# Kernel tuning notes

Measured on AMD Instinct MI355X. Metric: run time of the kernel, lower is better.

The kernel has to match this reference:

```python
import jax, jax.numpy as jnp
import numpy as np

B, L, D = 32, 2048, 512
DFF = D // 2          # FeedForward d_ff = d_model // 2
NBLK = 2 * 3          # head_number * block_layer sequential TX blocks
EPS = 1e-6


def _norm(x, alpha, bias):
    # torch Norm: alpha*(x-mean)/(std+eps)+bias, std unbiased (ddof=1)
    mu = x.mean(axis=-1, keepdims=True)
    var = ((x - mu) ** 2).sum(axis=-1, keepdims=True) / (x.shape[-1] - 1)
    return alpha * (x - mu) / (jnp.sqrt(var) + EPS) + bias


def setup_inputs() -> dict:
    key = jax.random.key(0)
    ks = jax.random.split(key, 8)
    q = jax.random.normal(ks[0], (B, D), dtype=jnp.float32)
    k = jax.random.normal(ks[1], (B, L, D), dtype=jnp.float32)
    v = jax.random.normal(ks[2], (B, L, D), dtype=jnp.float32)
    # FeedForward params per block, init std=0.001 as in source
    W1 = jax.random.normal(ks[3], (NBLK, D, DFF), dtype=jnp.float32) * 0.001
    b1 = jnp.zeros((NBLK, DFF), dtype=jnp.float32)
    W2 = jax.random.normal(ks[4], (NBLK, DFF, D), dtype=jnp.float32) * 0.001
    b2 = jnp.zeros((NBLK, D), dtype=jnp.float32)
    # Norm params (alpha=1, bias=0 at init)
    alpha1 = jnp.ones((NBLK, D), dtype=jnp.float32)
    bias1 = jnp.zeros((NBLK, D), dtype=jnp.float32)
    alpha2 = jnp.ones((NBLK, D), dtype=jnp.float32)
    bias2 = jnp.zeros((NBLK, D), dtype=jnp.float32)
    return {"q": q, "k": k, "v": v, "W1": W1, "b1": b1, "W2": W2, "b2": b2,
            "alpha1": alpha1, "bias1": bias1, "alpha2": alpha2, "bias2": bias2}


def reference(q, k, v, W1, b1, W2, b2, alpha1, bias1, alpha2, bias2):
    scale = 1.0 / jnp.sqrt(jnp.asarray(D, dtype=q.dtype))
    weights_list = []
    outs = []
    idx = 0
    for _head in range(2):
        for _layer in range(3):
            # attention: scores (B,L) = <q, k_l>/sqrt(D); output (B,D)
            scores = jnp.einsum('bd,bld->bl', q, k) * scale
            s = jax.nn.softmax(scores, axis=-1)
            A = jnp.einsum('bl,bld->bd', s, v)
            q_ = _norm(A + q, alpha1[idx], bias1[idx])
            ff = jax.nn.relu(q_ @ W1[idx] + b1[idx]) @ W2[idx] + b2[idx]
            q = _norm(q_ + ff, alpha2[idx], bias2[idx])
            weights_list.append(s)
            idx += 1
        outs.append(q)
    out = jnp.concatenate(outs, axis=-1)          # head_comb_mode='cat' -> (B, 2D)
    weights = jnp.stack(weights_list, axis=-1)    # (B, L, 6)
    return out, weights
```

## Files before the change

### kernel.cpp

```cpp
#include <hip/hip_runtime.h>

#define BB 32
#define LL 2048
#define DD 512
#define DFFN 256
#define NBLK 6
#define NCHUNK 32
#define CHUNK 64
#define NTHR 256
#define EPSV 1e-6f

typedef float v4f __attribute__((ext_vector_type(4)));
typedef unsigned v2u __attribute__((ext_vector_type(2)));

__device__ __forceinline__ float bflo(unsigned u){ return __uint_as_float(u << 16); }
__device__ __forceinline__ float bfhi(unsigned u){ return __uint_as_float(u & 0xFFFF0000u); }
__device__ __forceinline__ unsigned pack2bf(float lo, float hi){
  unsigned a = __float_as_uint(lo); a += 0x7FFFu + ((a >> 16) & 1u);
  unsigned b = __float_as_uint(hi); b += 0x7FFFu + ((b >> 16) & 1u);
  return (a >> 16) | (b & 0xFFFF0000u);
}

__device__ __forceinline__ float blk_sum(float v, volatile float* red){
  #pragma unroll
  for (int o = 32; o > 0; o >>= 1) v += __shfl_xor(v, o, 64);
  if ((threadIdx.x & 63) == 0) red[threadIdx.x >> 6] = v;
  __syncthreads();
  float r = red[0] + red[1] + red[2] + red[3];
  __syncthreads();
  return r;
}

__global__ __launch_bounds__(NTHR)
void k_prep(const float* __restrict__ kin, const float* __restrict__ vin,
            const float* __restrict__ qin,
            unsigned* __restrict__ kbf, unsigned* __restrict__ vbf,
            float* __restrict__ q_cur) {
  const int bid = blockIdx.x;
  if (bid < 65536) {
    const float* src = (bid < 32768) ? kin : vin;
    unsigned*    dst = (bid < 32768) ? kbf : vbf;
    const size_t g = (size_t)(bid & 32767) * NTHR + threadIdx.x;
    v4f f = __builtin_nontemporal_load((const v4f*)src + g);
    v2u o; o.x = pack2bf(f.x, f.y); o.y = pack2bf(f.z, f.w);
    *((v2u*)dst + g) = o;
  } else {
    const size_t g = (size_t)(bid - 65536) * NTHR + threadIdx.x;
    *((v4f*)q_cur + g) = *((const v4f*)qin + g);
  }
}

__global__ __launch_bounds__(NTHR)
void k_att(const unsigned short* __restrict__ kbf,
           const unsigned short* __restrict__ vbf,
           const float* __restrict__ q_cur,
           float* __restrict__ eplane,
           float* __restrict__ Zc,
           float* __restrict__ partialA) {
  const int tid  = threadIdx.x;
  const int bid  = blockIdx.x;
  const int b    = bid >> 5;
  const int c    = bid & 31;
  const int l0   = c * CHUNK;
  const int wave = tid >> 6;
  const int lane = tid & 63;

  __shared__ __align__(16) float q_lds[DD];
  __shared__ float s_lds[CHUNK];
  __shared__ __align__(16) float pa_lds[4*DD];

  q_lds[tid]       = q_cur[b*DD + tid];
  q_lds[tid + 256] = q_cur[b*DD + tid + 256];
  __syncthreads();

  const float scale = 0.04419417382415922f;
  const int rg = lane >> 3;
  const int j  = lane & 7;
  #pragma unroll
  for (int pass = 0; pass < 2; ++pass) {
    int lrow = wave*16 + pass*8 + rg;
    const unsigned* krow = (const unsigned*)(kbf + ((size_t)b*LL + l0 + lrow)*DD);
    float acc = 0.f;
    #pragma unroll
    for (int it = 0; it < 8; ++it) {
      uint4 kv = *((const uint4*)(krow + it*32 + j*4));
      const float4* qv = (const float4*)&q_lds[it*64 + j*8];
      float4 qa = qv[0], qb = qv[1];
      acc += bflo(kv.x)*qa.x + bfhi(kv.x)*qa.y
           + bflo(kv.y)*qa.z + bfhi(kv.y)*qa.w
           + bflo(kv.z)*qb.x + bfhi(kv.z)*qb.y
           + bflo(kv.w)*qb.z + bfhi(kv.w)*qb.w;
    }
    acc += __shfl_xor(acc, 1, 64);
    acc += __shfl_xor(acc, 2, 64);
    acc += __shfl_xor(acc, 4, 64);
    if (j == 0) {
      float e = __expf(acc * scale);
      s_lds[lrow] = e;
      eplane[(size_t)b*LL + l0 + lrow] = e;
    }
  }
  __syncthreads();

  if (wave == 0) {
    float z = s_lds[lane];
    #pragma unroll
    for (int o = 32; o > 0; o >>= 1) z += __shfl_xor(z, o, 64);
    if (lane == 0) Zc[(b << 5) + c] = z;
  }

  float a0=0,a1=0,a2=0,a3=0,a4=0,a5=0,a6=0,a7=0;
  const unsigned* vbase = (const unsigned*)(vbf + ((size_t)b*LL + l0 + wave*16)*DD) + lane*4;
  #pragma unroll 8
  for (int r = 0; r < 16; ++r) {
    float p = s_lds[wave*16 + r];
    uint4 vv = *((const uint4*)(vbase + (size_t)r*(DD/2)));
    a0 += p*bflo(vv.x); a1 += p*bfhi(vv.x);
    a2 += p*bflo(vv.y); a3 += p*bfhi(vv.y);
    a4 += p*bflo(vv.z); a5 += p*bfhi(vv.z);
    a6 += p*bflo(vv.w); a7 += p*bfhi(vv.w);
  }
  {
    float4* pw = (float4*)&pa_lds[wave*DD + lane*8];
    pw[0] = make_float4(a0,a1,a2,a3);
    pw[1] = make_float4(a4,a5,a6,a7);
  }
  __syncthreads();
  {
    float r0 = pa_lds[tid]     + pa_lds[DD+tid]     + pa_lds[2*DD+tid]     + pa_lds[3*DD+tid];
    float r1 = pa_lds[tid+256] + pa_lds[DD+tid+256] + pa_lds[2*DD+tid+256] + pa_lds[3*DD+tid+256];
    partialA[((size_t)c*BB + b)*DD + tid]       = r0;
    partialA[((size_t)c*BB + b)*DD + tid + 256] = r1;
  }
}

__global__ __launch_bounds__(NTHR)
void k_ffn(const float* __restrict__ Zc,
           const float* __restrict__ partialA,
           float* __restrict__ q_cur,
           const float* __restrict__ W1,
           const float* __restrict__ b1,
           const float* __restrict__ W2,
           const float* __restrict__ b2,
           const float* __restrict__ al1,
           const float* __restrict__ bi1,
           const float* __restrict__ al2,
           const float* __restrict__ bi2,
           float* __restrict__ out,
           float* __restrict__ Zinv_buf,
           int idx) {
  const int tid = threadIdx.x;
  const int b   = blockIdx.x;

  __shared__ __align__(16) float a_lds[DD];
  __shared__ float h_lds[DFFN];
  __shared__ float red[4];
  __shared__ float ZZ;

  if (tid < 64) {
    float z = (tid < 32) ? Zc[(b << 5) + tid] : 0.f;
    #pragma unroll
    for (int o = 16; o > 0; o >>= 1) z += __shfl_xor(z, o, 64);
    if (tid == 0) { float zi = 1.f / z; ZZ = zi; Zinv_buf[idx*BB + b] = zi; }
  }
  __syncthreads();
  const float zinv = ZZ;

  float x0 = q_cur[b*DD + tid];
  float x1 = q_cur[b*DD + tid + 256];
  {
    float s0 = 0.f, s1 = 0.f;
    #pragma unroll
    for (int cc = 0; cc < NCHUNK; ++cc) {
      s0 += partialA[((size_t)cc*BB + b)*DD + tid];
      s1 += partialA[((size_t)cc*BB + b)*DD + tid + 256];
    }
    x0 += s0 * zinv;
    x1 += s1 * zinv;
  }
  float s  = blk_sum(x0 + x1, red);
  float mu = s * (1.f/512.f);
  float d0 = x0 - mu, d1 = x1 - mu;
  float vs = blk_sum(d0*d0 + d1*d1, red);
  float rstd = 1.f / (sqrtf(vs * (1.f/511.f)) + EPSV);
  a_lds[tid]       = al1[idx*DD + tid]       * (d0*rstd) + bi1[idx*DD + tid];
  a_lds[tid + 256] = al1[idx*DD + tid + 256] * (d1*rstd) + bi1[idx*DD + tid + 256];
  __syncthreads();

  {
    const float* w1p = W1 + (size_t)idx*DD*DFFN + tid;
    float f0=0,f1=0,f2=0,f3=0;
    #pragma unroll 4
    for (int d = 0; d < DD; d += 4) {
      f0 += a_lds[d+0]*w1p[(size_t)(d+0)*DFFN];
      f1 += a_lds[d+1]*w1p[(size_t)(d+1)*DFFN];
      f2 += a_lds[d+2]*w1p[(size_t)(d+2)*DFFN];
      f3 += a_lds[d+3]*w1p[(size_t)(d+3)*DFFN];
    }
    float hv = (f0+f1)+(f2+f3) + b1[idx*DFFN + tid];
    h_lds[tid] = fmaxf(hv, 0.f);
  }
  __syncthreads();

  float y0 = 0.f, y1 = 0.f;
  #pragma unroll
  for (int e = 0; e < 2; ++e) {
    int d = tid + e*256;
    const float* w2p = W2 + (size_t)idx*DFFN*DD + d;
    float f0=0,f1=0,f2=0,f3=0;
    #pragma unroll 4
    for (int jj = 0; jj < DFFN; jj += 4) {
      f0 += h_lds[jj+0]*w2p[(size_t)(jj+0)*DD];
      f1 += h_lds[jj+1]*w2p[(size_t)(jj+1)*DD];
      f2 += h_lds[jj+2]*w2p[(size_t)(jj+2)*DD];
      f3 += h_lds[jj+3]*w2p[(size_t)(jj+3)*DD];
    }
    float ff = (f0+f1)+(f2+f3) + b2[idx*DD + d];
    float yv = a_lds[d] + ff;
    if (e == 0) y0 = yv; else y1 = yv;
  }
  float s2  = blk_sum(y0 + y1, red);
  float mu2 = s2 * (1.f/512.f);
  float e0 = y0 - mu2, e1 = y1 - mu2;
  float vs2 = blk_sum(e0*e0 + e1*e1, red);
  float rstd2 = 1.f / (sqrtf(vs2 * (1.f/511.f)) + EPSV);
  float qn0 = al2[idx*DD + tid]       * (e0*rstd2) + bi2[idx*DD + tid];
  float qn1 = al2[idx*DD + tid + 256] * (e1*rstd2) + bi2[idx*DD + tid + 256];
  q_cur[b*DD + tid]       = qn0;
  q_cur[b*DD + tid + 256] = qn1;
  if (idx == 2) {
    out[b*1024 + tid]       = qn0;
    out[b*1024 + tid + 256] = qn1;
  } else if (idx == 5) {
    out[b*1024 + 512 + tid]       = qn0;
    out[b*1024 + 512 + tid + 256] = qn1;
  }
}

__global__ __launch_bounds__(NTHR)
void k_wout(const float* __restrict__ eall,
            const float* __restrict__ Zinv_buf,
            float* __restrict__ wout) {
  const int g = blockIdx.x * NTHR + threadIdx.x;
  const int b = g >> 11;
  const int l = g & 2047;
  float p[6];
  #pragma unroll
  for (int i = 0; i < 6; ++i)
    p[i] = eall[((size_t)i*BB + b)*LL + l] * Zinv_buf[i*BB + b];
  float* w = wout + (size_t)g*6;
  *((float2*)(w + 0)) = make_float2(p[0], p[1]);
  *((float2*)(w + 2)) = make_float2(p[2], p[3]);
  *((float2*)(w + 4)) = make_float2(p[4], p[5]);
}

extern "C" void kernel_launch(void* const* d_in, const int* in_sizes, int n_in,
                              void* d_out, int out_size, void* d_ws, size_t ws_size,
                              hipStream_t stream) {
  const float* qin = (const float*)d_in[0];
  const float* kin = (const float*)d_in[1];
  const float* vin = (const float*)d_in[2];
  const float* W1  = (const float*)d_in[3];
  const float* b1  = (const float*)d_in[4];
  const float* W2  = (const float*)d_in[5];
  const float* b2  = (const float*)d_in[6];
  const float* al1 = (const float*)d_in[7];
  const float* bi1 = (const float*)d_in[8];
  const float* al2 = (const float*)d_in[9];
  const float* bi2 = (const float*)d_in[10];
  float* out  = (float*)d_out;
  float* wout = out + BB*2*DD;

  unsigned short* kbf = (unsigned short*)d_ws;
  unsigned short* vbf = kbf + (size_t)BB*LL*DD;
  float* fws      = (float*)(vbf + (size_t)BB*LL*DD);
  float* q_cur    = fws;
  float* Zc       = q_cur + BB*DD;
  float* Zinv_buf = Zc + BB*NCHUNK;
  float* eall     = Zinv_buf + NBLK*BB;
  float* partialA = eall + (size_t)NBLK*BB*LL;

  k_prep<<<dim3(65552), dim3(NTHR), 0, stream>>>(kin, vin, qin,
                                                 (unsigned*)kbf, (unsigned*)vbf, q_cur);
  for (int idx = 0; idx < NBLK; ++idx) {
    k_att<<<dim3(BB*NCHUNK), dim3(NTHR), 0, stream>>>(kbf, vbf, q_cur,
                                                      eall + (size_t)idx*BB*LL, Zc, partialA);
    k_ffn<<<dim3(BB), dim3(NTHR), 0, stream>>>(Zc, partialA, q_cur,
                                               W1, b1, W2, b2, al1, bi1, al2, bi2,
                                               out, Zinv_buf, idx);
  }
  k_wout<<<dim3(BB*LL/NTHR), dim3(NTHR), 0, stream>>>(eall, Zinv_buf, wout);
}
```

Baseline: 653.9 us.

## Fuse bf16 K/V conversion into first attention pass and widen FFN blocks

Removes the separate prep kernel: the first attention launch reads fp32 K and V directly, computes scores and the weighted V sum from them, and writes the bf16 copies as a side effect, so K/V are read once rather than twice in that step. The FFN kernel moves to 1024 threads and splits the W1 and W2 reductions across segments, with partial sums reduced through shared memory, to shorten the serial dot-product loops. The first block reads q from the input directly. The cost is a heavier first attention kernel and extra synchronisation inside the FFN.

```diff
diff --git a/kernel.cpp b/kernel.cpp
--- a/kernel.cpp
+++ b/kernel.cpp
@@ -8,10 +8,10 @@
 #define NCHUNK 32
 #define CHUNK 64
 #define NTHR 256
+#define FTHR 1024
 #define EPSV 1e-6f
 
 typedef float v4f __attribute__((ext_vector_type(4)));
-typedef unsigned v2u __attribute__((ext_vector_type(2)));
 
 __device__ __forceinline__ float bflo(unsigned u){ return __uint_as_float(u << 16); }
 __device__ __forceinline__ float bfhi(unsigned u){ return __uint_as_float(u & 0xFFFF0000u); }
@@ -21,32 +21,109 @@
   return (a >> 16) | (b & 0xFFFF0000u);
 }
 
-__device__ __forceinline__ float blk_sum(float v, volatile float* red){
+__device__ __forceinline__ float blk_sum16(float v, volatile float* red){
   #pragma unroll
   for (int o = 32; o > 0; o >>= 1) v += __shfl_xor(v, o, 64);
   if ((threadIdx.x & 63) == 0) red[threadIdx.x >> 6] = v;
   __syncthreads();
-  float r = red[0] + red[1] + red[2] + red[3];
+  float r = 0.f;
+  #pragma unroll
+  for (int i = 0; i < 16; ++i) r += red[i];
   __syncthreads();
   return r;
 }
 
 __global__ __launch_bounds__(NTHR)
-void k_prep(const float* __restrict__ kin, const float* __restrict__ vin,
-            const float* __restrict__ qin,
-            unsigned* __restrict__ kbf, unsigned* __restrict__ vbf,
-            float* __restrict__ q_cur) {
-  const int bid = blockIdx.x;
-  if (bid < 65536) {
-    const float* src = (bid < 32768) ? kin : vin;
-    unsigned*    dst = (bid < 32768) ? kbf : vbf;
-    const size_t g = (size_t)(bid & 32767) * NTHR + threadIdx.x;
-    v4f f = __builtin_nontemporal_load((const v4f*)src + g);
-    v2u o; o.x = pack2bf(f.x, f.y); o.y = pack2bf(f.z, f.w);
-    *((v2u*)dst + g) = o;
-  } else {
-    const size_t g = (size_t)(bid - 65536) * NTHR + threadIdx.x;
-    *((v4f*)q_cur + g) = *((const v4f*)qin + g);
+void k_att_first(const float* __restrict__ kin,
+                 const float* __restrict__ vin,
+                 const float* __restrict__ qin,
+                 unsigned* __restrict__ kbf,
+                 unsigned* __restrict__ vbf,
+                 float* __restrict__ eplane,
+                 float* __restrict__ Zc,
+                 float* __restrict__ partialA) {
+  const int tid  = threadIdx.x;
+  const int bid  = blockIdx.x;
+  const int b    = bid >> 5;
+  const int c    = bid & 31;
+  const int l0   = c * CHUNK;
+  const int wave = tid >> 6;
+  const int lane = tid & 63;
+
+  __shared__ __align__(16) float q_lds[DD];
+  __shared__ float s_lds[CHUNK];
+  __shared__ __align__(16) float pa_lds[4*DD];
+
+  q_lds[tid]       = qin[b*DD + tid];
+  q_lds[tid + 256] = qin[b*DD + tid + 256];
+  __syncthreads();
+
+  const float scale = 0.04419417382415922f;
+  const int rg = lane >> 3;
+  const int j  = lane & 7;
+  #pragma unroll
+  for (int pass = 0; pass < 2; ++pass) {
+    int lrow = wave*16 + pass*8 + rg;
+    const float* krow = kin + ((size_t)b*LL + l0 + lrow)*DD;
+    unsigned*   krowb = kbf + ((size_t)b*LL + l0 + lrow)*(DD/2);
+    float acc = 0.f;
+    #pragma unroll
+    for (int it = 0; it < 8; ++it) {
+      v4f fa = __builtin_nontemporal_load((const v4f*)(krow + it*64 + j*8));
+      v4f fb = __builtin_nontemporal_load((const v4f*)(krow + it*64 + j*8 + 4));
+      const float4* qv = (const float4*)&q_lds[it*64 + j*8];
+      float4 qa = qv[0], qb = qv[1];
+      acc += fa.x*qa.x + fa.y*qa.y + fa.z*qa.z + fa.w*qa.w
+           + fb.x*qb.x + fb.y*qb.y + fb.z*qb.z + fb.w*qb.w;
+      uint4 o;
+      o.x = pack2bf(fa.x, fa.y); o.y = pack2bf(fa.z, fa.w);
+      o.z = pack2bf(fb.x, fb.y); o.w = pack2bf(fb.z, fb.w);
+      *((uint4*)(krowb + it*32 + j*4)) = o;
+    }
+    acc += __shfl_xor(acc, 1, 64);
+    acc += __shfl_xor(acc, 2, 64);
+    acc += __shfl_xor(acc, 4, 64);
+    if (j == 0) {
+      float e = __expf(acc * scale);
+      s_lds[lrow] = e;
+      eplane[(size_t)b*LL + l0 + lrow] = e;
+    }
+  }
+  __syncthreads();
+
+  if (wave == 0) {
+    float z = s_lds[lane];
+    #pragma unroll
+    for (int o = 32; o > 0; o >>= 1) z += __shfl_xor(z, o, 64);
+    if (lane == 0) Zc[(b << 5) + c] = z;
+  }
+
+  float a0=0,a1=0,a2=0,a3=0,a4=0,a5=0,a6=0,a7=0;
+  const float* vbase = vin + ((size_t)b*LL + l0 + wave*16)*DD + lane*8;
+  unsigned*    vbfb  = vbf + ((size_t)b*LL + l0 + wave*16)*(DD/2) + lane*4;
+  #pragma unroll 4
+  for (int r = 0; r < 16; ++r) {
+    float p = s_lds[wave*16 + r];
+    v4f f0 = __builtin_nontemporal_load((const v4f*)(vbase + (size_t)r*DD));
+    v4f f1 = __builtin_nontemporal_load((const v4f*)(vbase + (size_t)r*DD + 4));
+    a0 += p*f0.x; a1 += p*f0.y; a2 += p*f0.z; a3 += p*f0.w;
+    a4 += p*f1.x; a5 += p*f1.y; a6 += p*f1.z; a7 += p*f1.w;
+    uint4 o;
+    o.x = pack2bf(f0.x, f0.y); o.y = pack2bf(f0.z, f0.w);
+    o.z = pack2bf(f1.x, f1.y); o.w = pack2bf(f1.z, f1.w);
+    *((uint4*)(vbfb + (size_t)r*(DD/2))) = o;
+  }
+  {
+    float4* pw = (float4*)&pa_lds[wave*DD + lane*8];
+    pw[0] = make_float4(a0,a1,a2,a3);
+    pw[1] = make_float4(a4,a5,a6,a7);
+  }
+  __syncthreads();
+  {
+    float r0 = pa_lds[tid]     + pa_lds[DD+tid]     + pa_lds[2*DD+tid]     + pa_lds[3*DD+tid];
+    float r1 = pa_lds[tid+256] + pa_lds[DD+tid+256] + pa_lds[2*DD+tid+256] + pa_lds[3*DD+tid+256];
+    partialA[((size_t)c*BB + b)*DD + tid]       = r0;
+    partialA[((size_t)c*BB + b)*DD + tid + 256] = r1;
   }
 }
 
@@ -134,9 +211,10 @@
   }
 }
 
-__global__ __launch_bounds__(NTHR)
+__global__ __launch_bounds__(FTHR)
 void k_ffn(const float* __restrict__ Zc,
            const float* __restrict__ partialA,
+           const float* __restrict__ qsrc,
            float* __restrict__ q_cur,
            const float* __restrict__ W1,
            const float* __restrict__ b1,
@@ -154,7 +232,8 @@
 
   __shared__ __align__(16) float a_lds[DD];
   __shared__ float h_lds[DFFN];
-  __shared__ float red[4];
+  __shared__ float stage[1024];
+  __shared__ float red[16];
   __shared__ float ZZ;
 
   if (tid < 64) {
@@ -166,74 +245,76 @@
   __syncthreads();
   const float zinv = ZZ;
 
-  float x0 = q_cur[b*DD + tid];
-  float x1 = q_cur[b*DD + tid + 256];
-  {
-    float s0 = 0.f, s1 = 0.f;
-    #pragma unroll
-    for (int cc = 0; cc < NCHUNK; ++cc) {
-      s0 += partialA[((size_t)cc*BB + b)*DD + tid];
-      s1 += partialA[((size_t)cc*BB + b)*DD + tid + 256];
-    }
-    x0 += s0 * zinv;
-    x1 += s1 * zinv;
-  }
-  float s  = blk_sum(x0 + x1, red);
+  float x = 0.f;
+  if (tid < DD) {
+    float sA = 0.f;
+    #pragma unroll
+    for (int cc = 0; cc < NCHUNK; ++cc)
+      sA += partialA[((size_t)cc*BB + b)*DD + tid];
+    x = qsrc[b*DD + tid] + sA * zinv;
+  }
+  float s  = blk_sum16(x, red);
   float mu = s * (1.f/512.f);
-  float d0 = x0 - mu, d1 = x1 - mu;
-  float vs = blk_sum(d0*d0 + d1*d1, red);
+  float d  = (tid < DD) ? (x - mu) : 0.f;
+  float vs = blk_sum16(d*d, red);
   float rstd = 1.f / (sqrtf(vs * (1.f/511.f)) + EPSV);
-  a_lds[tid]       = al1[idx*DD + tid]       * (d0*rstd) + bi1[idx*DD + tid];
-  a_lds[tid + 256] = al1[idx*DD + tid + 256] * (d1*rstd) + bi1[idx*DD + tid + 256];
-  __syncthreads();
-
-  {
-    const float* w1p = W1 + (size_t)idx*DD*DFFN + tid;
+  if (tid < DD)
+    a_lds[tid] = al1[idx*DD + tid] * (d*rstd) + bi1[idx*DD + tid];
+  __syncthreads();
+
+  {
+    const int f   = tid & 255;
+    const int seg = tid >> 8;
+    const float* w1p = W1 + (size_t)idx*DD*DFFN + f;
+    const int d0 = seg*128;
     float f0=0,f1=0,f2=0,f3=0;
-    #pragma unroll 4
-    for (int d = 0; d < DD; d += 4) {
-      f0 += a_lds[d+0]*w1p[(size_t)(d+0)*DFFN];
-      f1 += a_lds[d+1]*w1p[(size_t)(d+1)*DFFN];
-      f2 += a_lds[d+2]*w1p[(size_t)(d+2)*DFFN];
-      f3 += a_lds[d+3]*w1p[(size_t)(d+3)*DFFN];
-    }
-    float hv = (f0+f1)+(f2+f3) + b1[idx*DFFN + tid];
+    #pragma unroll 8
+    for (int dd = d0; dd < d0+128; dd += 4) {
+      f0 += a_lds[dd+0]*w1p[(size_t)(dd+0)*DFFN];
+      f1 += a_lds[dd+1]*w1p[(size_t)(dd+1)*DFFN];
+      f2 += a_lds[dd+2]*w1p[(size_t)(dd+2)*DFFN];
+      f3 += a_lds[dd+3]*w1p[(size_t)(dd+3)*DFFN];
+    }
+    stage[seg*256 + f] = (f0+f1)+(f2+f3);
+  }
+  __syncthreads();
+  if (tid < DFFN) {
+    float hv = stage[tid] + stage[256+tid] + stage[512+tid] + stage[768+tid]
+             + b1[idx*DFFN + tid];
     h_lds[tid] = fmaxf(hv, 0.f);
   }
   __syncthreads();
 
-  float y0 = 0.f, y1 = 0.f;
-  #pragma unroll
-  for (int e = 0; e < 2; ++e) {
-    int d = tid + e*256;
-    const float* w2p = W2 + (size_t)idx*DFFN*DD + d;
+  {
+    const int dout = tid & 511;
+    const int seg2 = tid >> 9;
+    const float* w2p = W2 + (size_t)idx*DFFN*DD + dout;
+    const int j0 = seg2*128;
     float f0=0,f1=0,f2=0,f3=0;
-    #pragma unroll 4
-    for (int jj = 0; jj < DFFN; jj += 4) {
+    #pragma unroll 8
+    for (int jj = j0; jj < j0+128; jj += 4) {
       f0 += h_lds[jj+0]*w2p[(size_t)(jj+0)*DD];
       f1 += h_lds[jj+1]*w2p[(size_t)(jj+1)*DD];
       f2 += h_lds[jj+2]*w2p[(size_t)(jj+2)*DD];
       f3 += h_lds[jj+3]*w2p[(size_t)(jj+3)*DD];
     }
-    float ff = (f0+f1)+(f2+f3) + b2[idx*DD + d];
-    float yv = a_lds[d] + ff;
-    if (e == 0) y0 = yv; else y1 = yv;
-  }
-  float s2  = blk_sum(y0 + y1, red);
+    stage[seg2*512 + dout] = (f0+f1)+(f2+f3);
+  }
+  __syncthreads();
+
+  float y = 0.f;
+  if (tid < DD)
+    y = a_lds[tid] + stage[tid] + stage[512+tid] + b2[idx*DD + tid];
+  float s2  = blk_sum16(y, red);
   float mu2 = s2 * (1.f/512.f);
-  float e0 = y0 - mu2, e1 = y1 - mu2;
-  float vs2 = blk_sum(e0*e0 + e1*e1, red);
+  float e   = (tid < DD) ? (y - mu2) : 0.f;
+  float vs2 = blk_sum16(e*e, red);
   float rstd2 = 1.f / (sqrtf(vs2 * (1.f/511.f)) + EPSV);
-  float qn0 = al2[idx*DD + tid]       * (e0*rstd2) + bi2[idx*DD + tid];
-  float qn1 = al2[idx*DD + tid + 256] * (e1*rstd2) + bi2[idx*DD + tid + 256];
-  q_cur[b*DD + tid]       = qn0;
-  q_cur[b*DD + tid + 256] = qn1;
-  if (idx == 2) {
-    out[b*1024 + tid]       = qn0;
-    out[b*1024 + tid + 256] = qn1;
-  } else if (idx == 5) {
-    out[b*1024 + 512 + tid]       = qn0;
-    out[b*1024 + 512 + tid + 256] = qn1;
+  if (tid < DD) {
+    float qn = al2[idx*DD + tid] * (e*rstd2) + bi2[idx*DD + tid];
+    q_cur[b*DD + tid] = qn;
+    if (idx == 2)      out[b*1024 + tid]       = qn;
+    else if (idx == 5) out[b*1024 + 512 + tid] = qn;
   }
 }
 
@@ -280,12 +361,17 @@
   float* eall     = Zinv_buf + NBLK*BB;
   float* partialA = eall + (size_t)NBLK*BB*LL;
 
-  k_prep<<<dim3(65552), dim3(NTHR), 0, stream>>>(kin, vin, qin,
-                                                 (unsigned*)kbf, (unsigned*)vbf, q_cur);
   for (int idx = 0; idx < NBLK; ++idx) {
-    k_att<<<dim3(BB*NCHUNK), dim3(NTHR), 0, stream>>>(kbf, vbf, q_cur,
-                                                      eall + (size_t)idx*BB*LL, Zc, partialA);
-    k_ffn<<<dim3(BB), dim3(NTHR), 0, stream>>>(Zc, partialA, q_cur,
+    if (idx == 0) {
+      k_att_first<<<dim3(BB*NCHUNK), dim3(NTHR), 0, stream>>>(
+          kin, vin, qin, (unsigned*)kbf, (unsigned*)vbf,
+          eall, Zc, partialA);
+    } else {
+      k_att<<<dim3(BB*NCHUNK), dim3(NTHR), 0, stream>>>(
+          kbf, vbf, q_cur, eall + (size_t)idx*BB*LL, Zc, partialA);
+    }
+    const float* qsrc = (idx == 0) ? qin : q_cur;
+    k_ffn<<<dim3(BB), dim3(FTHR), 0, stream>>>(Zc, partialA, qsrc, q_cur,
                                                W1, b1, W2, b2, al1, bi1, al2, bi2,
                                                out, Zinv_buf, idx);
   }
```

New measurement: 548.2 us. -16.2%, faster.
